# Performance work log

Hardware: AMD Instinct MI355X
Metric: run time of the kernel (lower is better)

The kernel has to match this reference:

```python
import jax, jax.numpy as jnp
import numpy as np

BN_EPS = 1e-5

def conv1x1(t, w, b):
    # t: [B,Cin,H,W], w: [Cout,Cin], b: [Cout]
    return jnp.einsum('bchw,oc->bohw', t, w) + b[None, :, None, None]

def setup_inputs() -> dict:
    key = jax.random.key(0)
    ks = jax.random.split(key, 11)
    B, Cx, Hx, Wx = 8, 64, 128, 64
    Cy, Hy, Wy = 256, 64, 32
    d = Cy // 8  # num_heads=8
    return {
        'x': jax.random.normal(ks[0], (B, Cx, Hx, Wx), jnp.float32),
        'y': jax.random.normal(ks[1], (B, Cy, Hy, Wy), jnp.float32),
        'wq': jax.random.normal(ks[2], (d, Cy), jnp.float32) * 0.05,
        'bq': jax.random.normal(ks[3], (d,), jnp.float32) * 0.05,
        'wk': jax.random.normal(ks[4], (d, Cy), jnp.float32) * 0.05,
        'bk': jax.random.normal(ks[5], (d,), jnp.float32) * 0.05,
        'wv': jax.random.normal(ks[6], (Cx, Cx), jnp.float32) * 0.05,
        'bv': jax.random.normal(ks[7], (Cx,), jnp.float32) * 0.05,
        'gamma': jax.random.normal(ks[8], (1,), jnp.float32),
        'bn_w': jax.random.normal(ks[9], (Cx,), jnp.float32),
        'bn_b': jax.random.normal(ks[10], (Cx,), jnp.float32),
    }

def reference(x, y, wq, bq, wk, bk, wv, bv, gamma, bn_w, bn_b):
    B, Cx, Hx, Wx = x.shape
    _, Cy, Hy, Wy = y.shape
    size_x = Hx * Wx
    size_y = Hy * Wy
    r = size_x // size_y  # nearest-upsample replication factor (integer here)

    q = conv1x1(y, wq, bq).reshape(B, -1, size_y)  # [B,d,Sy]
    k = conv1x1(y, wk, bk).reshape(B, -1, size_y)  # [B,d,Sy]
    energy = jnp.einsum('bds,bdt->bst', q, k)      # [B,Sy,Sy]
    A = jax.nn.softmax(energy, axis=-1)            # [B,Sy,Sy]

    v = conv1x1(x, wv, bv).reshape(B, Cx, size_x)  # [B,Cx,Sx]
    # Nearest upsample of A to [Sx,Sx] with A_up[i,j]=A[i//r, j//r], then
    # out[c,i] = sum_j v[c,j]*A_up[i,j]  ==  repeat( v_pooled @ A^T , r )
    v_pool = v.reshape(B, Cx, size_y, r).sum(-1)   # block-sum over j within each low-res bin
    O = jnp.einsum('bcj,bij->bci', v_pool, A)      # [B,Cx,Sy]
    out = jnp.repeat(O, r, axis=-1)                # replicate along i: index i -> i//r
    out = out.reshape(B, Cx, Hx, Wx)

    out = gamma[0] * out
    # BatchNorm2d (training-mode batch statistics, biased variance)
    mean = out.mean(axis=(0, 2, 3), keepdims=True)
    var = out.var(axis=(0, 2, 3), keepdims=True)
    out = (out - mean) * jax.lax.rsqrt(var + BN_EPS)
    out = out * bn_w[None, :, None, None] + bn_b[None, :, None, None]
    return x + out
```

## Files before the change

### kernel.cpp

```cpp
#include <hip/hip_runtime.h>
#include <hip/hip_bf16.h>

typedef __attribute__((ext_vector_type(8))) short short8;
typedef __attribute__((ext_vector_type(4))) float f32x4;
typedef unsigned short ushort_t;
typedef unsigned int uint_t;

static constexpr int B  = 8;
static constexpr int CX = 64;
static constexpr int SX = 8192;
static constexpr int CY = 256;
static constexpr int SY = 2048;
static constexpr int D  = 32;

static constexpr size_t OFF_Q  = 0;
static constexpr size_t OFF_K  = OFF_Q + (size_t)B*SY*D*2;
static constexpr size_t OFF_V  = OFF_K + (size_t)B*SY*D*2;
static constexpr size_t OFF_O  = OFF_V + (size_t)B*CX*SY*2;
static constexpr size_t OFF_P1 = OFF_O + (size_t)B*CX*SY*4;
static constexpr size_t OFF_P2 = OFF_P1 + 512*64*4;
static constexpr size_t OFF_SC = OFF_P2 + 512*64*4;
static constexpr size_t OFF_SH = OFF_SC + 64*4;

__device__ inline ushort_t f2bf(float f) {
    uint_t u = __builtin_bit_cast(uint_t, f);
    u += 0x7fffu + ((u >> 16) & 1u);
    return (ushort_t)(u >> 16);
}
__device__ inline uint_t pack_bf16(float a, float b) {
    uint_t ua = __builtin_bit_cast(uint_t, a);
    uint_t ub = __builtin_bit_cast(uint_t, b);
    ua += 0x7fffu + ((ua >> 16) & 1u);
    ub += 0x7fffu + ((ub >> 16) & 1u);
    return (ua >> 16) | (ub & 0xffff0000u);
}

__global__ __launch_bounds__(1024) void k_qk(
    const float* __restrict__ y, const float* __restrict__ wq,
    const float* __restrict__ bq, const float* __restrict__ wk,
    const float* __restrict__ bk, ushort_t* __restrict__ qT, ushort_t* __restrict__ kT)
{
    __shared__ __align__(16) unsigned char Wl[32768];
    __shared__ __align__(16) unsigned char Yl[32768];
    const int t  = threadIdx.x;
    const int b  = blockIdx.x >> 5;
    const int s0 = (blockIdx.x & 31) << 6;

#pragma unroll
    for (int p = 0; p < 8; ++p) {
        const int idx = p * 1024 + t;
        const int o   = idx >> 7;
        const int c2  = idx & 127;
        const float f0 = (o < 32) ? wq[o * CY + 2 * c2]     : wk[(o - 32) * CY + 2 * c2];
        const float f1 = (o < 32) ? wq[o * CY + 2 * c2 + 1] : wk[(o - 32) * CY + 2 * c2 + 1];
        *reinterpret_cast<uint_t*>(Wl + ((o * 512 + c2 * 4) ^ ((o & 7) << 4))) = pack_bf16(f0, f1);
    }
    {
        const int l = t & 63, cg = t >> 6;
        const float* ysrc = y + (size_t)(b * CY + cg * 16) * SY + s0 + l;
#pragma unroll
        for (int k = 0; k < 8; ++k) {
            const float f0 = ysrc[(2 * k)     * SY];
            const float f1 = ysrc[(2 * k + 1) * SY];
            const int c = cg * 16 + 2 * k;
            *reinterpret_cast<uint_t*>(Yl + ((l * 512 + c * 2) ^ ((l & 7) << 4))) = pack_bf16(f0, f1);
        }
    }
    __syncthreads();

    const int w  = t >> 6, l = t & 63;
    const int li = l & 15, g = l >> 4;
    const int ot = w & 3,  st = w >> 2;
    const int oo = ot * 16 + li;
    const int ss = st * 16 + li;

    f32x4 acc = (f32x4){0.f, 0.f, 0.f, 0.f};
#pragma unroll
    for (int ch = 0; ch < 8; ++ch) {
        const short8 wf = *reinterpret_cast<const short8*>(
            Wl + ((oo * 512 + ch * 64 + g * 16) ^ ((oo & 7) << 4)));
        const short8 yf = *reinterpret_cast<const short8*>(
            Yl + ((ss * 512 + ch * 64 + g * 16) ^ ((ss & 7) << 4)));
        acc = __builtin_amdgcn_mfma_f32_16x16x32_bf16(wf, yf, acc, 0, 0, 0);
    }
    const float* bias = (ot < 2) ? bq : bk;
    const int ob = (ot & 1) * 16 + g * 4;
    const float v0 = acc[0] + bias[ob + 0];
    const float v1 = acc[1] + bias[ob + 1];
    const float v2 = acc[2] + bias[ob + 2];
    const float v3 = acc[3] + bias[ob + 3];
    uint2 pw; pw.x = pack_bf16(v0, v1); pw.y = pack_bf16(v2, v3);
    ushort_t* dst = (ot < 2) ? qT : kT;
    *reinterpret_cast<uint2*>(dst + (size_t)(b * SY + s0 + ss) * D + ob) = pw;
}

__global__ __launch_bounds__(1024) void k_v(
    const float* __restrict__ x, const float* __restrict__ wv,
    const float* __restrict__ bv, ushort_t* __restrict__ vB)
{
    __shared__ __align__(16) float xp[64][68];
    __shared__ __align__(16) float wt[64][68];
    const int t   = threadIdx.x;
    const int b   = blockIdx.x >> 5;
    const int jj0 = (blockIdx.x & 31) << 6;

#pragma unroll
    for (int p = 0; p < 4; ++p) {
        const int f = p * 1024 + t;
        const int co = f >> 6, ci = f & 63;
        wt[ci][co] = wv[co * 64 + ci];
    }
    {
        const float4* x4 = reinterpret_cast<const float4*>(x);
#pragma unroll
        for (int p = 0; p < 4; ++p) {
            const int f = p * 1024 + t;
            const int ci = f >> 6, j = f & 63;
            const float4 v = x4[(size_t)(b * CX + ci) * (SX / 4) + jj0 + j];
            xp[ci][j] = (v.x + v.y) + (v.z + v.w);
        }
    }
    __syncthreads();

    const int w = t >> 6, j = t & 63;
    float a0 = 0.f, a1 = 0.f, a2 = 0.f, a3 = 0.f;
#pragma unroll 4
    for (int ci = 0; ci < 64; ++ci) {
        const float xv = xp[ci][j];
        const float4 w4 = *reinterpret_cast<const float4*>(&wt[ci][w * 4]);
        a0 += w4.x * xv; a1 += w4.y * xv; a2 += w4.z * xv; a3 += w4.w * xv;
    }
    const int c0 = w * 4;
    const size_t base = (size_t)(b * CX) * SY + jj0 + j;
    vB[base + (size_t)(c0 + 0) * SY] = f2bf(a0 + 4.f * bv[c0 + 0]);
    vB[base + (size_t)(c0 + 1) * SY] = f2bf(a1 + 4.f * bv[c0 + 1]);
    vB[base + (size_t)(c0 + 2) * SY] = f2bf(a2 + 4.f * bv[c0 + 2]);
    vB[base + (size_t)(c0 + 3) * SY] = f2bf(a3 + 4.f * bv[c0 + 3]);
}

__global__ __launch_bounds__(1024) void k_attn(
    const ushort_t* __restrict__ qT, const ushort_t* __restrict__ kT,
    const ushort_t* __restrict__ vB, float* __restrict__ O,
    float* __restrict__ part1, float* __restrict__ part2)
{
    __shared__ __align__(16) unsigned char smem[69632];
    unsigned char* Kb0 = smem;
    unsigned char* Kb1 = smem + 8192;
    unsigned char* Vb0 = smem + 16384;
    unsigned char* Vb1 = smem + 32768;
    unsigned char* Pw  = smem + 49152;
    float* Otile = reinterpret_cast<float*>(smem);
    float* Lpart = reinterpret_cast<float*>(smem + 17408);
    float* invL  = reinterpret_cast<float*>(smem + 18432);

    const int t  = threadIdx.x;
    const int w  = t >> 6, l = t & 63;
    const int g  = l >> 4, li = l & 15;
    const int b  = blockIdx.x >> 5;
    const int i0 = (blockIdx.x & 31) << 6;

    const int m  = w & 3;
    const int jq = w >> 2;

    const ushort_t* kb = kT + (size_t)b * SY * D;
    const ushort_t* vb = vB + (size_t)b * CX * SY;

    const short8 qf = *reinterpret_cast<const short8*>(
        qT + ((size_t)(b * SY + i0 + m * 16 + li)) * D + g * 8);

    const int koff = w * 1024 + l * 16;
    const int vc = w * 4 + g;
    const int vldso = vc * 256 + li * 16;
    const unsigned char* kgb = reinterpret_cast<const unsigned char*>(kb);
    const unsigned char* vgb = reinterpret_cast<const unsigned char*>(vb)
                             + (size_t)vc * (SY * 2) + ((li ^ (vc & 7)) * 16);

    unsigned char* Pme = Pw + w * 1280;
    const int swzV = (li & 7) << 4;

    f32x4 acc[4];
#pragma unroll
    for (int n = 0; n < 4; ++n) acc[n] = (f32x4){0.f, 0.f, 0.f, 0.f};
    float lsum = 0.f;

    {
        short8 kr, vr;
        if (w < 8) kr = *reinterpret_cast<const short8*>(kgb + koff);
        vr = *reinterpret_cast<const short8*>(vgb);
        if (w < 8) *reinterpret_cast<short8*>(Kb0 + koff) = kr;
        *reinterpret_cast<short8*>(Vb0 + vldso) = vr;
    }
    __syncthreads();

    for (int ch = 0; ch < 16; ++ch) {
        unsigned char* Kc = (ch & 1) ? Kb1 : Kb0;
        unsigned char* Vc = (ch & 1) ? Vb1 : Vb0;
        unsigned char* Kn = (ch & 1) ? Kb0 : Kb1;
        unsigned char* Vn = (ch & 1) ? Vb0 : Vb1;

        short8 kr, vr;
        if (ch < 15) {
            if (w < 8) kr = *reinterpret_cast<const short8*>(kgb + (size_t)(ch + 1) * 8192 + koff);
            vr = *reinterpret_cast<const short8*>(vgb + (size_t)(ch + 1) * 256);
        }

        const short8 kf0 = *reinterpret_cast<const short8*>(Kc + (jq * 32 + li) * 64 + g * 16);
        const short8 kf1 = *reinterpret_cast<const short8*>(Kc + (jq * 32 + 16 + li) * 64 + g * 16);
        const f32x4 d0 = __builtin_amdgcn_mfma_f32_16x16x32_bf16(kf0, qf, (f32x4){0.f,0.f,0.f,0.f}, 0, 0, 0);
        const f32x4 d1 = __builtin_amdgcn_mfma_f32_16x16x32_bf16(kf1, qf, (f32x4){0.f,0.f,0.f,0.f}, 0, 0, 0);

        {
            const float e0 = __expf(d0[0]), e1 = __expf(d0[1]);
            const float e2 = __expf(d0[2]), e3 = __expf(d0[3]);
            const float h0 = __expf(d1[0]), h1 = __expf(d1[1]);
            const float h2 = __expf(d1[2]), h3 = __expf(d1[3]);
            lsum += ((e0 + e1) + (e2 + e3)) + ((h0 + h1) + (h2 + h3));
            uint2 p0; p0.x = pack_bf16(e0, e1); p0.y = pack_bf16(e2, e3);
            *reinterpret_cast<uint2*>(Pme + li * 80 + 8 * g) = p0;
            uint2 p1; p1.x = pack_bf16(h0, h1); p1.y = pack_bf16(h2, h3);
            *reinterpret_cast<uint2*>(Pme + li * 80 + 32 + 8 * g) = p1;
        }

        const short8 pf = *reinterpret_cast<const short8*>(Pme + li * 80 + 16 * g);
#pragma unroll
        for (int n = 0; n < 4; ++n) {
            const short8 vf = *reinterpret_cast<const short8*>(
                Vc + (n * 16 + li) * 256 + ((jq * 64 + g * 16) ^ swzV));
            acc[n] = __builtin_amdgcn_mfma_f32_16x16x32_bf16(pf, vf, acc[n], 0, 0, 0);
        }

        if (ch < 15) {
            if (w < 8) *reinterpret_cast<short8*>(Kn + koff) = kr;
            *reinterpret_cast<short8*>(Vn + vldso) = vr;
        }
        __syncthreads();
    }

    lsum += __shfl_xor(lsum, 16, 64);
    lsum += __shfl_xor(lsum, 32, 64);
    if (l < 16) Lpart[jq * 64 + m * 16 + l] = lsum;

    if (jq == 0) {
#pragma unroll
        for (int n = 0; n < 4; ++n) {
            *reinterpret_cast<float4*>(&Otile[(n * 16 + li) * 68 + m * 16 + g * 4]) =
                make_float4(acc[n][0], acc[n][1], acc[n][2], acc[n][3]);
        }
    }
    __syncthreads();
    if (t < 64) {
        float L = 0.f;
#pragma unroll
        for (int jj = 0; jj < 4; ++jj) L += Lpart[jj * 64 + t];
        invL[t] = 1.f / L;
    }
    if (jq == 1) {
#pragma unroll
        for (int n = 0; n < 4; ++n) {
            float4* p = reinterpret_cast<float4*>(&Otile[(n * 16 + li) * 68 + m * 16 + g * 4]);
            float4 v = *p;
            v.x += acc[n][0]; v.y += acc[n][1]; v.z += acc[n][2]; v.w += acc[n][3];
            *p = v;
        }
    }
    __syncthreads();
    if (jq == 2) {
#pragma unroll
        for (int n = 0; n < 4; ++n) {
            float4* p = reinterpret_cast<float4*>(&Otile[(n * 16 + li) * 68 + m * 16 + g * 4]);
            float4 v = *p;
            v.x += acc[n][0]; v.y += acc[n][1]; v.z += acc[n][2]; v.w += acc[n][3];
            *p = v;
        }
    }
    __syncthreads();
    if (jq == 3) {
#pragma unroll
        for (int n = 0; n < 4; ++n) {
            float4* p = reinterpret_cast<float4*>(&Otile[(n * 16 + li) * 68 + m * 16 + g * 4]);
            float4 v = *p;
            v.x += acc[n][0]; v.y += acc[n][1]; v.z += acc[n][2]; v.w += acc[n][3];
            *p = v;
        }
    }
    __syncthreads();

    if (t < 64) {
        float sa = 0.f, sq = 0.f;
        for (int i = 0; i < 64; ++i) {
            const float v = Otile[t * 68 + i] * invL[i];
            sa += v; sq += v * v;
        }
        part1[blockIdx.x * 64 + t] = sa;
        part2[blockIdx.x * 64 + t] = sq;
    }

    {
        const int c = t >> 4, i4 = t & 15;
        float4 o;
        o.x = Otile[c * 68 + i4 * 4 + 0] * invL[i4 * 4 + 0];
        o.y = Otile[c * 68 + i4 * 4 + 1] * invL[i4 * 4 + 1];
        o.z = Otile[c * 68 + i4 * 4 + 2] * invL[i4 * 4 + 2];
        o.w = Otile[c * 68 + i4 * 4 + 3] * invL[i4 * 4 + 3];
        reinterpret_cast<float4*>(O)[(size_t)(b * CX + c) * (SY / 4) + (i0 >> 2) + i4] = o;
    }
}

__global__ __launch_bounds__(1024) void k_bn(
    const float* __restrict__ part1, const float* __restrict__ part2,
    const float* __restrict__ gamma, const float* __restrict__ bn_w,
    const float* __restrict__ bn_b, float* __restrict__ sc,
    float* __restrict__ sh)
{
    __shared__ float r1[16][64], r2[16][64];
    const int t = threadIdx.x;
    const int c = t & 63, q = t >> 6;
    float s1 = 0.f, s2 = 0.f;
#pragma unroll
    for (int n = 0; n < 16; ++n) {
        const int row = n * 16 + q;
        s1 += part1[row * 64 + c];
        s2 += part2[row * 64 + c];
    }
    r1[q][c] = s1; r2[q][c] = s2;
    __syncthreads();
    if (t < 64) {
        float S1 = 0.f, S2 = 0.f;
#pragma unroll
        for (int k = 0; k < 16; ++k) { S1 += r1[k][t]; S2 += r2[k][t]; }
        const float g = gamma[0];
        const float invN = 1.f / 16384.f;
        const float mean = S1 * invN;
        const float var  = S2 * invN - mean * mean;
        const float inv  = rsqrtf(g * g * var + 1e-5f);
        const float scale = g * inv * bn_w[t];
        sc[t] = scale;
        sh[t] = bn_b[t] - mean * scale;
    }
}

__global__ __launch_bounds__(256) void k_out(
    const float* __restrict__ x, const float* __restrict__ Obuf,
    const float* __restrict__ sc, const float* __restrict__ sh,
    float* __restrict__ out)
{
    const int gid = blockIdx.x * 256 + threadIdx.x;
    const int c = (gid >> 11) & 63;
    const float o  = Obuf[gid];
    const float4 xv = reinterpret_cast<const float4*>(x)[gid];
    const float val = o * sc[c] + sh[c];
    float4 r;
    r.x = xv.x + val; r.y = xv.y + val; r.z = xv.z + val; r.w = xv.w + val;
    reinterpret_cast<float4*>(out)[gid] = r;
}

extern "C" void kernel_launch(void* const* d_in, const int* in_sizes, int n_in,
                              void* d_out, int out_size, void* d_ws, size_t ws_size,
                              hipStream_t stream)
{
    (void)in_sizes; (void)n_in; (void)out_size; (void)ws_size;
    const float* x  = (const float*)d_in[0];
    const float* y  = (const float*)d_in[1];
    const float* wq = (const float*)d_in[2];
    const float* bq = (const float*)d_in[3];
    const float* wk = (const float*)d_in[4];
    const float* bk = (const float*)d_in[5];
    const float* wv = (const float*)d_in[6];
    const float* bv = (const float*)d_in[7];
    const float* gm = (const float*)d_in[8];
    const float* bw = (const float*)d_in[9];
    const float* bb = (const float*)d_in[10];

    char* ws = (char*)d_ws;
    ushort_t* qT  = (ushort_t*)(ws + OFF_Q);
    ushort_t* kT  = (ushort_t*)(ws + OFF_K);
    ushort_t* vBp = (ushort_t*)(ws + OFF_V);
    float*    Ob  = (float*)(ws + OFF_O);
    float*    p1  = (float*)(ws + OFF_P1);
    float*    p2  = (float*)(ws + OFF_P2);
    float*    scp = (float*)(ws + OFF_SC);
    float*    shp = (float*)(ws + OFF_SH);

    k_qk  <<<256, 1024, 0, stream>>>(y, wq, bq, wk, bk, qT, kT);
    k_v   <<<256, 1024, 0, stream>>>(x, wv, bv, vBp);
    k_attn<<<256, 1024, 0, stream>>>(qT, kT, vBp, Ob, p1, p2);
    k_bn  <<<1,   1024, 0, stream>>>(p1, p2, gm, bw, bb, scp, shp);
    k_out <<<4096, 256, 0, stream>>>(x, Ob, scp, shp, (float*)d_out);
}
```

Baseline: 131.0 us.

## Merge QK and V projection kernels; load K fragments directly from global

```diff
diff --git a/kernel.cpp b/kernel.cpp
--- a/kernel.cpp
+++ b/kernel.cpp
@@ -35,107 +35,108 @@
     return (ua >> 16) | (ub & 0xffff0000u);
 }
 
-__global__ __launch_bounds__(1024) void k_qk(
+__global__ __launch_bounds__(1024) void k_prod(
     const float* __restrict__ y, const float* __restrict__ wq,
     const float* __restrict__ bq, const float* __restrict__ wk,
-    const float* __restrict__ bk, ushort_t* __restrict__ qT, ushort_t* __restrict__ kT)
-{
-    __shared__ __align__(16) unsigned char Wl[32768];
-    __shared__ __align__(16) unsigned char Yl[32768];
-    const int t  = threadIdx.x;
-    const int b  = blockIdx.x >> 5;
-    const int s0 = (blockIdx.x & 31) << 6;
-
-#pragma unroll
-    for (int p = 0; p < 8; ++p) {
-        const int idx = p * 1024 + t;
-        const int o   = idx >> 7;
-        const int c2  = idx & 127;
-        const float f0 = (o < 32) ? wq[o * CY + 2 * c2]     : wk[(o - 32) * CY + 2 * c2];
-        const float f1 = (o < 32) ? wq[o * CY + 2 * c2 + 1] : wk[(o - 32) * CY + 2 * c2 + 1];
-        *reinterpret_cast<uint_t*>(Wl + ((o * 512 + c2 * 4) ^ ((o & 7) << 4))) = pack_bf16(f0, f1);
-    }
-    {
-        const int l = t & 63, cg = t >> 6;
-        const float* ysrc = y + (size_t)(b * CY + cg * 16) * SY + s0 + l;
-#pragma unroll
-        for (int k = 0; k < 8; ++k) {
-            const float f0 = ysrc[(2 * k)     * SY];
-            const float f1 = ysrc[(2 * k + 1) * SY];
-            const int c = cg * 16 + 2 * k;
-            *reinterpret_cast<uint_t*>(Yl + ((l * 512 + c * 2) ^ ((l & 7) << 4))) = pack_bf16(f0, f1);
-        }
-    }
-    __syncthreads();
-
-    const int w  = t >> 6, l = t & 63;
-    const int li = l & 15, g = l >> 4;
-    const int ot = w & 3,  st = w >> 2;
-    const int oo = ot * 16 + li;
-    const int ss = st * 16 + li;
-
-    f32x4 acc = (f32x4){0.f, 0.f, 0.f, 0.f};
-#pragma unroll
-    for (int ch = 0; ch < 8; ++ch) {
-        const short8 wf = *reinterpret_cast<const short8*>(
-            Wl + ((oo * 512 + ch * 64 + g * 16) ^ ((oo & 7) << 4)));
-        const short8 yf = *reinterpret_cast<const short8*>(
-            Yl + ((ss * 512 + ch * 64 + g * 16) ^ ((ss & 7) << 4)));
-        acc = __builtin_amdgcn_mfma_f32_16x16x32_bf16(wf, yf, acc, 0, 0, 0);
-    }
-    const float* bias = (ot < 2) ? bq : bk;
-    const int ob = (ot & 1) * 16 + g * 4;
-    const float v0 = acc[0] + bias[ob + 0];
-    const float v1 = acc[1] + bias[ob + 1];
-    const float v2 = acc[2] + bias[ob + 2];
-    const float v3 = acc[3] + bias[ob + 3];
-    uint2 pw; pw.x = pack_bf16(v0, v1); pw.y = pack_bf16(v2, v3);
-    ushort_t* dst = (ot < 2) ? qT : kT;
-    *reinterpret_cast<uint2*>(dst + (size_t)(b * SY + s0 + ss) * D + ob) = pw;
-}
-
-__global__ __launch_bounds__(1024) void k_v(
+    const float* __restrict__ bk, ushort_t* __restrict__ qT, ushort_t* __restrict__ kT,
     const float* __restrict__ x, const float* __restrict__ wv,
     const float* __restrict__ bv, ushort_t* __restrict__ vB)
 {
-    __shared__ __align__(16) float xp[64][68];
-    __shared__ __align__(16) float wt[64][68];
-    const int t   = threadIdx.x;
-    const int b   = blockIdx.x >> 5;
-    const int jj0 = (blockIdx.x & 31) << 6;
-
-#pragma unroll
-    for (int p = 0; p < 4; ++p) {
-        const int f = p * 1024 + t;
-        const int co = f >> 6, ci = f & 63;
-        wt[ci][co] = wv[co * 64 + ci];
-    }
-    {
-        const float4* x4 = reinterpret_cast<const float4*>(x);
+    __shared__ __align__(16) unsigned char lds[65536];
+    const int t = threadIdx.x;
+
+    if (blockIdx.x < 256) {
+        unsigned char* Wl = lds;
+        unsigned char* Yl = lds + 32768;
+        const int b  = blockIdx.x >> 5;
+        const int s0 = (blockIdx.x & 31) << 6;
+
+#pragma unroll
+        for (int p = 0; p < 8; ++p) {
+            const int idx = p * 1024 + t;
+            const int o   = idx >> 7;
+            const int c2  = idx & 127;
+            const float f0 = (o < 32) ? wq[o * CY + 2 * c2]     : wk[(o - 32) * CY + 2 * c2];
+            const float f1 = (o < 32) ? wq[o * CY + 2 * c2 + 1] : wk[(o - 32) * CY + 2 * c2 + 1];
+            *reinterpret_cast<uint_t*>(Wl + ((o * 512 + c2 * 4) ^ ((o & 7) << 4))) = pack_bf16(f0, f1);
+        }
+        {
+            const int l = t & 63, cg = t >> 6;
+            const float* ysrc = y + (size_t)(b * CY + cg * 16) * SY + s0 + l;
+#pragma unroll
+            for (int k = 0; k < 8; ++k) {
+                const float f0 = ysrc[(2 * k)     * SY];
+                const float f1 = ysrc[(2 * k + 1) * SY];
+                const int c = cg * 16 + 2 * k;
+                *reinterpret_cast<uint_t*>(Yl + ((l * 512 + c * 2) ^ ((l & 7) << 4))) = pack_bf16(f0, f1);
+            }
+        }
+        __syncthreads();
+
+        const int w  = t >> 6, l = t & 63;
+        const int li = l & 15, g = l >> 4;
+        const int ot = w & 3,  st = w >> 2;
+        const int oo = ot * 16 + li;
+        const int ss = st * 16 + li;
+
+        f32x4 acc = (f32x4){0.f, 0.f, 0.f, 0.f};
+#pragma unroll
+        for (int ch = 0; ch < 8; ++ch) {
+            const short8 wf = *reinterpret_cast<const short8*>(
+                Wl + ((oo * 512 + ch * 64 + g * 16) ^ ((oo & 7) << 4)));
+            const short8 yf = *reinterpret_cast<const short8*>(
+                Yl + ((ss * 512 + ch * 64 + g * 16) ^ ((ss & 7) << 4)));
+            acc = __builtin_amdgcn_mfma_f32_16x16x32_bf16(wf, yf, acc, 0, 0, 0);
+        }
+        const float* bias = (ot < 2) ? bq : bk;
+        const int ob = (ot & 1) * 16 + g * 4;
+        const float v0 = acc[0] + bias[ob + 0];
+        const float v1 = acc[1] + bias[ob + 1];
+        const float v2 = acc[2] + bias[ob + 2];
+        const float v3 = acc[3] + bias[ob + 3];
+        uint2 pw; pw.x = pack_bf16(v0, v1); pw.y = pack_bf16(v2, v3);
+        ushort_t* dst = (ot < 2) ? qT : kT;
+        *reinterpret_cast<uint2*>(dst + (size_t)(b * SY + s0 + ss) * D + ob) = pw;
+    } else {
+        float* xp = reinterpret_cast<float*>(lds);
+        float* wt = reinterpret_cast<float*>(lds + 17408);
+        const int bid = blockIdx.x - 256;
+        const int b   = bid >> 5;
+        const int jj0 = (bid & 31) << 6;
+
 #pragma unroll
         for (int p = 0; p < 4; ++p) {
             const int f = p * 1024 + t;
-            const int ci = f >> 6, j = f & 63;
-            const float4 v = x4[(size_t)(b * CX + ci) * (SX / 4) + jj0 + j];
-            xp[ci][j] = (v.x + v.y) + (v.z + v.w);
-        }
-    }
-    __syncthreads();
-
-    const int w = t >> 6, j = t & 63;
-    float a0 = 0.f, a1 = 0.f, a2 = 0.f, a3 = 0.f;
+            const int co = f >> 6, ci = f & 63;
+            wt[ci * 68 + co] = wv[co * 64 + ci];
+        }
+        {
+            const float4* x4 = reinterpret_cast<const float4*>(x);
+#pragma unroll
+            for (int p = 0; p < 4; ++p) {
+                const int f = p * 1024 + t;
+                const int ci = f >> 6, j = f & 63;
+                const float4 v = x4[(size_t)(b * CX + ci) * (SX / 4) + jj0 + j];
+                xp[ci * 68 + j] = (v.x + v.y) + (v.z + v.w);
+            }
+        }
+        __syncthreads();
+
+        const int w = t >> 6, j = t & 63;
+        float a0 = 0.f, a1 = 0.f, a2 = 0.f, a3 = 0.f;
 #pragma unroll 4
-    for (int ci = 0; ci < 64; ++ci) {
-        const float xv = xp[ci][j];
-        const float4 w4 = *reinterpret_cast<const float4*>(&wt[ci][w * 4]);
-        a0 += w4.x * xv; a1 += w4.y * xv; a2 += w4.z * xv; a3 += w4.w * xv;
-    }
-    const int c0 = w * 4;
-    const size_t base = (size_t)(b * CX) * SY + jj0 + j;
-    vB[base + (size_t)(c0 + 0) * SY] = f2bf(a0 + 4.f * bv[c0 + 0]);
-    vB[base + (size_t)(c0 + 1) * SY] = f2bf(a1 + 4.f * bv[c0 + 1]);
-    vB[base + (size_t)(c0 + 2) * SY] = f2bf(a2 + 4.f * bv[c0 + 2]);
-    vB[base + (size_t)(c0 + 3) * SY] = f2bf(a3 + 4.f * bv[c0 + 3]);
+        for (int ci = 0; ci < 64; ++ci) {
+            const float xv = xp[ci * 68 + j];
+            const float4 w4 = *reinterpret_cast<const float4*>(&wt[ci * 68 + w * 4]);
+            a0 += w4.x * xv; a1 += w4.y * xv; a2 += w4.z * xv; a3 += w4.w * xv;
+        }
+        const int c0 = w * 4;
+        const size_t base = (size_t)(b * CX) * SY + jj0 + j;
+        vB[base + (size_t)(c0 + 0) * SY] = f2bf(a0 + 4.f * bv[c0 + 0]);
+        vB[base + (size_t)(c0 + 1) * SY] = f2bf(a1 + 4.f * bv[c0 + 1]);
+        vB[base + (size_t)(c0 + 2) * SY] = f2bf(a2 + 4.f * bv[c0 + 2]);
+        vB[base + (size_t)(c0 + 3) * SY] = f2bf(a3 + 4.f * bv[c0 + 3]);
+    }
 }
 
 __global__ __launch_bounds__(1024) void k_attn(
@@ -143,12 +144,10 @@
     const ushort_t* __restrict__ vB, float* __restrict__ O,
     float* __restrict__ part1, float* __restrict__ part2)
 {
-    __shared__ __align__(16) unsigned char smem[69632];
-    unsigned char* Kb0 = smem;
-    unsigned char* Kb1 = smem + 8192;
-    unsigned char* Vb0 = smem + 16384;
-    unsigned char* Vb1 = smem + 32768;
-    unsigned char* Pw  = smem + 49152;
+    __shared__ __align__(16) unsigned char smem[53248];
+    unsigned char* Vb0 = smem;
+    unsigned char* Vb1 = smem + 16384;
+    unsigned char* Pw  = smem + 32768;
     float* Otile = reinterpret_cast<float*>(smem);
     float* Lpart = reinterpret_cast<float*>(smem + 17408);
     float* invL  = reinterpret_cast<float*>(smem + 18432);
@@ -168,10 +167,10 @@
     const short8 qf = *reinterpret_cast<const short8*>(
         qT + ((size_t)(b * SY + i0 + m * 16 + li)) * D + g * 8);
 
-    const int koff = w * 1024 + l * 16;
+    const unsigned char* kgb = reinterpret_cast<const unsigned char*>(kb)
+                             + (jq * 32 + li) * 64 + g * 16;
     const int vc = w * 4 + g;
     const int vldso = vc * 256 + li * 16;
-    const unsigned char* kgb = reinterpret_cast<const unsigned char*>(kb);
     const unsigned char* vgb = reinterpret_cast<const unsigned char*>(vb)
                              + (size_t)vc * (SY * 2) + ((li ^ (vc & 7)) * 16);
 
@@ -183,31 +182,27 @@
     for (int n = 0; n < 4; ++n) acc[n] = (f32x4){0.f, 0.f, 0.f, 0.f};
     float lsum = 0.f;
 
+    short8 kc0 = *reinterpret_cast<const short8*>(kgb);
+    short8 kc1 = *reinterpret_cast<const short8*>(kgb + 16 * 64);
     {
-        short8 kr, vr;
-        if (w < 8) kr = *reinterpret_cast<const short8*>(kgb + koff);
-        vr = *reinterpret_cast<const short8*>(vgb);
-        if (w < 8) *reinterpret_cast<short8*>(Kb0 + koff) = kr;
+        const short8 vr = *reinterpret_cast<const short8*>(vgb);
         *reinterpret_cast<short8*>(Vb0 + vldso) = vr;
     }
     __syncthreads();
 
     for (int ch = 0; ch < 16; ++ch) {
-        unsigned char* Kc = (ch & 1) ? Kb1 : Kb0;
         unsigned char* Vc = (ch & 1) ? Vb1 : Vb0;
-        unsigned char* Kn = (ch & 1) ? Kb0 : Kb1;
         unsigned char* Vn = (ch & 1) ? Vb0 : Vb1;
 
-        short8 kr, vr;
+        short8 kn0, kn1, vr;
         if (ch < 15) {
-            if (w < 8) kr = *reinterpret_cast<const short8*>(kgb + (size_t)(ch + 1) * 8192 + koff);
-            vr = *reinterpret_cast<const short8*>(vgb + (size_t)(ch + 1) * 256);
-        }
-
-        const short8 kf0 = *reinterpret_cast<const short8*>(Kc + (jq * 32 + li) * 64 + g * 16);
-        const short8 kf1 = *reinterpret_cast<const short8*>(Kc + (jq * 32 + 16 + li) * 64 + g * 16);
-        const f32x4 d0 = __builtin_amdgcn_mfma_f32_16x16x32_bf16(kf0, qf, (f32x4){0.f,0.f,0.f,0.f}, 0, 0, 0);
-        const f32x4 d1 = __builtin_amdgcn_mfma_f32_16x16x32_bf16(kf1, qf, (f32x4){0.f,0.f,0.f,0.f}, 0, 0, 0);
+            kn0 = *reinterpret_cast<const short8*>(kgb + (size_t)(ch + 1) * 8192);
+            kn1 = *reinterpret_cast<const short8*>(kgb + (size_t)(ch + 1) * 8192 + 1024);
+            vr  = *reinterpret_cast<const short8*>(vgb + (size_t)(ch + 1) * 256);
+        }
+
+        const f32x4 d0 = __builtin_amdgcn_mfma_f32_16x16x32_bf16(kc0, qf, (f32x4){0.f,0.f,0.f,0.f}, 0, 0, 0);
+        const f32x4 d1 = __builtin_amdgcn_mfma_f32_16x16x32_bf16(kc1, qf, (f32x4){0.f,0.f,0.f,0.f}, 0, 0, 0);
 
         {
             const float e0 = __expf(d0[0]), e1 = __expf(d0[1]);
@@ -230,10 +225,10 @@
         }
 
         if (ch < 15) {
-            if (w < 8) *reinterpret_cast<short8*>(Kn + koff) = kr;
             *reinterpret_cast<short8*>(Vn + vldso) = vr;
         }
         __syncthreads();
+        kc0 = kn0; kc1 = kn1;
     }
 
     lsum += __shfl_xor(lsum, 16, 64);
@@ -381,8 +376,7 @@
     float*    scp = (float*)(ws + OFF_SC);
     float*    shp = (float*)(ws + OFF_SH);
 
-    k_qk  <<<256, 1024, 0, stream>>>(y, wq, bq, wk, bk, qT, kT);
-    k_v   <<<256, 1024, 0, stream>>>(x, wv, bv, vBp);
+    k_prod<<<512, 1024, 0, stream>>>(y, wq, bq, wk, bk, qT, kT, x, wv, bv, vBp);
     k_attn<<<256, 1024, 0, stream>>>(qT, kT, vBp, Ob, p1, p2);
     k_bn  <<<1,   1024, 0, stream>>>(p1, p2, gm, bw, bb, scp, shp);
     k_out <<<4096, 256, 0, stream>>>(x, Ob, scp, shp, (float*)d_out);
```

New measurement: 126.2 us. 1.04x faster.
